# Optimization experiments

Hardware: AMD Instinct MI355X
Metric: run time of the kernel (lower is better)

## Reference

```python
import jax, jax.numpy as jnp
import numpy as np

N, E = 50000, 600000
DIMS = [128, 256, 256, 256, 256, 64]  # in, h1..h4, out


def setup_inputs() -> dict:
    key = jax.random.key(0)
    ks = jax.random.split(key, 12)
    inp = {
        "x": jax.random.normal(ks[0], (N, DIMS[0]), dtype=jnp.float32),
        "edge_index": jax.random.randint(ks[1], (2, E), 0, N, dtype=jnp.int64 if jax.config.jax_enable_x64 else jnp.int32),
    }
    for i in range(5):
        fi, fo = DIMS[i], DIMS[i + 1]
        s = 1.0 / np.sqrt(fi)  # glorot-ish uniform, matching GCNConv default scale
        inp[f"W{i+1}"] = jax.random.uniform(ks[2 + 2 * i], (fi, fo), jnp.float32, -s, s)
        inp[f"b{i+1}"] = jnp.zeros((fo,), jnp.float32)
    return inp


def _gcn_norm(edge_index, n):
    # Add self-loops and compute symmetric normalization D^-1/2 (A+I) D^-1/2.
    loop = jnp.arange(n, dtype=edge_index.dtype)
    src = jnp.concatenate([edge_index[0], loop])  # [E+N]
    dst = jnp.concatenate([edge_index[1], loop])
    deg = jax.ops.segment_sum(jnp.ones_like(dst, dtype=jnp.float32), dst, num_segments=n)
    dinv = jnp.where(deg > 0, jax.lax.rsqrt(deg), 0.0)
    norm = dinv[src] * dinv[dst]  # [E+N]
    return src, dst, norm


def _gcn_layer(x, src, dst, norm, W, b, n):
    h = x @ W                       # [N, Fo] linear transform first (fewer msg bytes)
    msg = h[src] * norm[:, None]    # gather + edge-weight scale
    out = jax.ops.segment_sum(msg, dst, num_segments=n)  # scatter-add aggregate
    return out + b


def reference(x, edge_index, W1, b1, W2, b2, W3, b3, W4, b4, W5, b5):
    n = x.shape[0]
    src, dst, norm = _gcn_norm(edge_index, n)
    params = [(W1, b1), (W2, b2), (W3, b3), (W4, b4), (W5, b5)]
    h = x
    for i, (W, b) in enumerate(params):
        h = _gcn_layer(h, src, dst, norm, W, b, n)
        if i < 4:
            h = jax.nn.relu(h)  # dropout is identity in eval mode
    return h
```

## Files before the change

kernel.cpp:

```cpp
#include <hip/hip_runtime.h>
#include <stdint.h>


typedef _Float16 v8h __attribute__((ext_vector_type(8)));
typedef float v4f __attribute__((ext_vector_type(4)));

__global__ void count_edges(const int* __restrict__ dst, int E, int* __restrict__ counts) {
    int i = blockIdx.x * blockDim.x + threadIdx.x;
    if (i < E) atomicAdd(&counts[dst[i]], 1);
}

__global__ void block_sums(const int* __restrict__ counts, int n, int* __restrict__ partial) {
    __shared__ int red[256];
    int t = threadIdx.x;
    int i = blockIdx.x * 256 + t;
    red[t] = (i < n) ? counts[i] : 0;
    __syncthreads();
    #pragma unroll
    for (int off = 128; off > 0; off >>= 1) {
        if (t < off) red[t] += red[t + off];
        __syncthreads();
    }
    if (t == 0) partial[blockIdx.x] = red[0];
}

__global__ void scan_partials(int* __restrict__ partial, int nb, int* __restrict__ row_ptr, int n) {
    __shared__ int s[256];
    int t = threadIdx.x;
    int v = (t < nb) ? partial[t] : 0;
    s[t] = v;
    __syncthreads();
    #pragma unroll
    for (int off = 1; off < 256; off <<= 1) {
        int u = (t >= off) ? s[t - off] : 0;
        __syncthreads();
        s[t] += u;
        __syncthreads();
    }
    if (t < nb) partial[t] = s[t] - v;
    if (t == 0) row_ptr[n] = s[255];
}

__global__ void scan_final(const int* __restrict__ counts, int n, const int* __restrict__ partial,
                           int* __restrict__ row_ptr, float* __restrict__ dinv,
                           int* __restrict__ fill) {
    __shared__ int s[256];
    int t = threadIdx.x;
    int i = blockIdx.x * 256 + t;
    int c = (i < n) ? counts[i] : 0;
    s[t] = c;
    __syncthreads();
    #pragma unroll
    for (int off = 1; off < 256; off <<= 1) {
        int u = (t >= off) ? s[t - off] : 0;
        __syncthreads();
        s[t] += u;
        __syncthreads();
    }
    if (i < n) {
        row_ptr[i] = partial[blockIdx.x] + s[t] - c;
        dinv[i] = rsqrtf((float)(c + 1));
        fill[i] = 0;
    }
}

__global__ void build_csr(const int* __restrict__ src, const int* __restrict__ dst, int E,
                          const int* __restrict__ row_ptr, int* __restrict__ fill,
                          int* __restrict__ ssrc, float* __restrict__ wsrc,
                          const float* __restrict__ dinv) {
    int i = blockIdx.x * blockDim.x + threadIdx.x;
    if (i < E) {
        int d = dst[i];
        int s = src[i];
        int pos = row_ptr[d] + atomicAdd(&fill[d], 1);
        ssrc[pos] = s;
        wsrc[pos] = dinv[s];
    }
}

struct SplitArgs {
    const float* W[5];
    _Float16* Wh[5];
    _Float16* Wl[5];
    int lgFI[5];
    int FO[5];
    int off[6];
};

__global__ void split_all(SplitArgs a) {
    int i = blockIdx.x * 256 + threadIdx.x;
    #pragma unroll
    for (int l = 0; l < 5; ++l) {
        if (i >= a.off[l] && i < a.off[l + 1]) {
            int j = i - a.off[l];
            int FI = 1 << a.lgFI[l];
            int c = j >> a.lgFI[l];
            int k = j & (FI - 1);
            float v = a.W[l][(size_t)k * a.FO[l] + c];
            _Float16 h = (_Float16)v;
            a.Wh[l][j] = h;
            a.Wl[l][j] = (_Float16)(v - (float)h);
        }
    }
}

template <int F, bool SPLIT_OUT>
__global__ void agg_f32(const float* __restrict__ in, const int* __restrict__ row_ptr,
                        const int* __restrict__ ssrc, const float* __restrict__ wsrc,
                        const float* __restrict__ dinv, const float* __restrict__ bias,
                        _Float16* __restrict__ outH, _Float16* __restrict__ outL,
                        float* __restrict__ outF, int n) {
    constexpr int VE = F / 64;
    int wid = (blockIdx.x * blockDim.x + threadIdx.x) >> 6;
    if (wid >= n) return;
    int lane = threadIdx.x & 63;
    const float dd = dinv[wid];
    float acc[VE];

    auto loadrow = [&](int row, float* v) {
        if constexpr (VE == 2) {
            float2 t = *(const float2*)&in[(size_t)row * F + lane * 2];
            v[0] = t.x; v[1] = t.y;
        } else {
            v[0] = in[(size_t)row * F + lane];
        }
    };

    {
        float v[VE];
        loadrow(wid, v);
        #pragma unroll
        for (int j = 0; j < VE; ++j) acc[j] = dd * v[j];
    }
    int e = row_ptr[wid];
    const int end = row_ptr[wid + 1];
    for (; e + 4 <= end; e += 4) {
        int s0 = ssrc[e], s1 = ssrc[e + 1], s2 = ssrc[e + 2], s3 = ssrc[e + 3];
        float w0 = wsrc[e], w1 = wsrc[e + 1], w2 = wsrc[e + 2], w3 = wsrc[e + 3];
        float v0[VE], v1[VE], v2[VE], v3[VE];
        loadrow(s0, v0); loadrow(s1, v1); loadrow(s2, v2); loadrow(s3, v3);
        #pragma unroll
        for (int j = 0; j < VE; ++j) acc[j] += w0 * v0[j] + w1 * v1[j];
        #pragma unroll
        for (int j = 0; j < VE; ++j) acc[j] += w2 * v2[j] + w3 * v3[j];
    }
    for (; e < end; ++e) {
        int s = ssrc[e];
        float w = wsrc[e];
        float v[VE];
        loadrow(s, v);
        #pragma unroll
        for (int j = 0; j < VE; ++j) acc[j] += w * v[j];
    }

    if constexpr (SPLIT_OUT) {
        size_t o = (size_t)wid * F + lane * VE;
        #pragma unroll
        for (int j = 0; j < VE; ++j) {
            float s = dd * acc[j];
            _Float16 h = (_Float16)s;
            outH[o + j] = h;
            outL[o + j] = (_Float16)(s - (float)h);
        }
    } else {
        #pragma unroll
        for (int j = 0; j < VE; ++j) {
            float s = dd * acc[j] + bias[lane * VE + j];
            outF[(size_t)wid * F + lane * VE + j] = s;
        }
    }
}

__global__ void agg_packed(const _Float16* __restrict__ inP, const int* __restrict__ row_ptr,
                           const int* __restrict__ ssrc, const float* __restrict__ wsrc,
                           const float* __restrict__ dinv,
                           _Float16* __restrict__ outH, _Float16* __restrict__ outL, int n) {
    int wid = (blockIdx.x * blockDim.x + threadIdx.x) >> 6;
    if (wid >= n) return;
    int lane = threadIdx.x & 63;
    const float dd = dinv[wid];
    float acc[4];

    auto loadrow = [&](int row, float* v) {
        v8h p = *(const v8h*)&inP[(size_t)row * 512 + lane * 8];
        v[0] = (float)p[0] + (float)p[1];
        v[1] = (float)p[2] + (float)p[3];
        v[2] = (float)p[4] + (float)p[5];
        v[3] = (float)p[6] + (float)p[7];
    };

    {
        float v[4];
        loadrow(wid, v);
        #pragma unroll
        for (int j = 0; j < 4; ++j) acc[j] = dd * v[j];
    }
    int e = row_ptr[wid];
    const int end = row_ptr[wid + 1];
    for (; e + 4 <= end; e += 4) {
        int s0 = ssrc[e], s1 = ssrc[e + 1], s2 = ssrc[e + 2], s3 = ssrc[e + 3];
        float w0 = wsrc[e], w1 = wsrc[e + 1], w2 = wsrc[e + 2], w3 = wsrc[e + 3];
        float v0[4], v1[4], v2[4], v3[4];
        loadrow(s0, v0); loadrow(s1, v1); loadrow(s2, v2); loadrow(s3, v3);
        #pragma unroll
        for (int j = 0; j < 4; ++j) acc[j] += w0 * v0[j] + w1 * v1[j];
        #pragma unroll
        for (int j = 0; j < 4; ++j) acc[j] += w2 * v2[j] + w3 * v3[j];
    }
    for (; e < end; ++e) {
        int s = ssrc[e];
        float w = wsrc[e];
        float v[4];
        loadrow(s, v);
        #pragma unroll
        for (int j = 0; j < 4; ++j) acc[j] += w * v[j];
    }

    size_t o = (size_t)wid * 256 + lane * 4;
    #pragma unroll
    for (int j = 0; j < 4; ++j) {
        float s = dd * acc[j];
        _Float16 h = (_Float16)s;
        outH[o + j] = h;
        outL[o + j] = (_Float16)(s - (float)h);
    }
}

__device__ __forceinline__ void gl_lds16(const _Float16* g, _Float16* l) {
    __builtin_amdgcn_global_load_lds(
        (const __attribute__((address_space(1))) uint32_t*)g,
        (__attribute__((address_space(3))) uint32_t*)l, 16, 0, 0);
}

template <int FI, int OUTMODE>
__global__ __launch_bounds__(256) void gemm_wide(
    const _Float16* __restrict__ Ah, const _Float16* __restrict__ Al,
    const _Float16* __restrict__ Wth, const _Float16* __restrict__ Wtl,
    const float* __restrict__ bias,
    uint32_t* __restrict__ Opk, _Float16* __restrict__ Oh, _Float16* __restrict__ Ol,
    int n) {
    constexpr int BK = 32;
    constexpr int NSTEP = FI / BK;
    __shared__ _Float16 lds[20480];
    const int m0 = blockIdx.x * 64;
    const int t = threadIdx.x;
    const int w = t >> 6;
    const int lane = t & 63;

    const int G = w * 64 + lane;
    const int arow = (G >> 6) * 16 + (G & 15), akc = ((G >> 4) & 3) * 8;
    const _Float16* sAh = Ah + (size_t)(m0 + arow) * FI + akc;
    const _Float16* sAl = Al + (size_t)(m0 + arow) * FI + akc;
    _Float16* dAh = &lds[w * 512];
    _Float16* dAl = &lds[2048 + w * 512];
    const int bq = lane & 15, bk = (lane >> 4) * 8;
    const _Float16* sB[4];
    _Float16* dBh[4];
    _Float16* dBl[4];
    #pragma unroll
    for (int q = 0; q < 4; ++q) {
        int sub = w * 4 + q;
        sB[q] = (const _Float16*)((size_t)(sub * 16 + bq) * FI + bk);
        dBh[q] = &lds[4096 + sub * 512];
        dBl[q] = &lds[12288 + sub * 512];
    }

    v4f acc[4][4];
    #pragma unroll
    for (int i = 0; i < 4; ++i)
        #pragma unroll
        for (int j = 0; j < 4; ++j) acc[i][j] = (v4f){0.f, 0.f, 0.f, 0.f};

    for (int s = 0; s < NSTEP; ++s) {
        const int ko = s * BK;
        gl_lds16(sAh + ko, dAh);
        gl_lds16(sAl + ko, dAl);
        #pragma unroll
        for (int q = 0; q < 4; ++q) {
            size_t off = (size_t)sB[q];
            gl_lds16(Wth + off + ko, dBh[q]);
            gl_lds16(Wtl + off + ko, dBl[q]);
        }
        __syncthreads();
        v8h ahf[4], alf[4], bhf[4], blf[4];
        #pragma unroll
        for (int i = 0; i < 4; ++i) {
            ahf[i] = *(const v8h*)&lds[i * 512 + lane * 8];
            alf[i] = *(const v8h*)&lds[2048 + i * 512 + lane * 8];
        }
        #pragma unroll
        for (int j = 0; j < 4; ++j) {
            bhf[j] = *(const v8h*)&lds[4096 + (w * 4 + j) * 512 + lane * 8];
            blf[j] = *(const v8h*)&lds[12288 + (w * 4 + j) * 512 + lane * 8];
        }
        #pragma unroll
        for (int i = 0; i < 4; ++i)
            #pragma unroll
            for (int j = 0; j < 4; ++j) {
                acc[i][j] = __builtin_amdgcn_mfma_f32_16x16x32_f16(ahf[i], bhf[j], acc[i][j], 0, 0, 0);
                acc[i][j] = __builtin_amdgcn_mfma_f32_16x16x32_f16(ahf[i], blf[j], acc[i][j], 0, 0, 0);
                acc[i][j] = __builtin_amdgcn_mfma_f32_16x16x32_f16(alf[i], bhf[j], acc[i][j], 0, 0, 0);
            }
        __syncthreads();
    }

    const int rl = (lane >> 4) * 4;
    const int cl = lane & 15;
    #pragma unroll
    for (int j = 0; j < 4; ++j) {
        const int gcol = w * 64 + j * 16 + cl;
        const float bv = bias[gcol];
        #pragma unroll
        for (int i = 0; i < 4; ++i) {
            const int grow = m0 + i * 16 + rl;
            #pragma unroll
            for (int r = 0; r < 4; ++r) {
                if (grow + r < n) {
                    float v = fmaxf(acc[i][j][r] + bv, 0.f);
                    _Float16 h = (_Float16)v;
                    _Float16 l = (_Float16)(v - (float)h);
                    if (OUTMODE == 0) {
                        uint32_t u = (uint32_t)__builtin_bit_cast(uint16_t, h) |
                                     ((uint32_t)__builtin_bit_cast(uint16_t, l) << 16);
                        Opk[(size_t)(grow + r) * 256 + gcol] = u;
                    } else {
                        Oh[(size_t)(grow + r) * 256 + gcol] = h;
                        Ol[(size_t)(grow + r) * 256 + gcol] = l;
                    }
                }
            }
        }
    }
}

__global__ __launch_bounds__(256) void gemm_narrow(
    const _Float16* __restrict__ Ah, const _Float16* __restrict__ Al,
    const _Float16* __restrict__ Wth, const _Float16* __restrict__ Wtl,
    float* __restrict__ Of, int n) {
    constexpr int FI = 256, FO = 64;
    __shared__ _Float16 lds[12288];
    const int m0 = blockIdx.x * 128;
    const int t = threadIdx.x;
    const int w = t >> 6;
    const int lane = t & 63;

    const int G0 = w * 128 + lane;
    const int G1 = G0 + 64;
    const int arow0 = (G0 >> 6) * 16 + (G0 & 15), akc0 = ((G0 >> 4) & 3) * 8;
    const int arow1 = (G1 >> 6) * 16 + (G1 & 15), akc1 = ((G1 >> 4) & 3) * 8;
    const _Float16* sAh0 = Ah + (size_t)(m0 + arow0) * FI + akc0;
    const _Float16* sAh1 = Ah + (size_t)(m0 + arow1) * FI + akc1;
    const _Float16* sAl0 = Al + (size_t)(m0 + arow0) * FI + akc0;
    const _Float16* sAl1 = Al + (size_t)(m0 + arow1) * FI + akc1;
    const int bcol = w * 16 + (lane & 15), bkc = (lane >> 4) * 8;
    const _Float16* sBh = Wth + (size_t)bcol * FI + bkc;
    const _Float16* sBl = Wtl + (size_t)bcol * FI + bkc;

    _Float16* dAh0 = &lds[w * 1024];
    _Float16* dAh1 = &lds[w * 1024 + 512];
    _Float16* dAl0 = &lds[4096 + w * 1024];
    _Float16* dAl1 = &lds[4096 + w * 1024 + 512];
    _Float16* dBh = &lds[8192 + w * 512];
    _Float16* dBl = &lds[10240 + w * 512];

    const int wm = w >> 1, wn = w & 1;
    v4f acc[4][2];
    #pragma unroll
    for (int i = 0; i < 4; ++i)
        #pragma unroll
        for (int j = 0; j < 2; ++j) acc[i][j] = (v4f){0.f, 0.f, 0.f, 0.f};

    for (int s = 0; s < 8; ++s) {
        const int ko = s * 32;
        gl_lds16(sAh0 + ko, dAh0);
        gl_lds16(sAh1 + ko, dAh1);
        gl_lds16(sAl0 + ko, dAl0);
        gl_lds16(sAl1 + ko, dAl1);
        gl_lds16(sBh + ko, dBh);
        gl_lds16(sBl + ko, dBl);
        __syncthreads();
        v8h ah[4], al[4], bh[2], bl[2];
        #pragma unroll
        for (int i = 0; i < 4; ++i) {
            ah[i] = *(const v8h*)&lds[(wm * 4 + i) * 512 + lane * 8];
            al[i] = *(const v8h*)&lds[4096 + (wm * 4 + i) * 512 + lane * 8];
        }
        #pragma unroll
        for (int j = 0; j < 2; ++j) {
            bh[j] = *(const v8h*)&lds[8192 + (wn * 2 + j) * 512 + lane * 8];
            bl[j] = *(const v8h*)&lds[10240 + (wn * 2 + j) * 512 + lane * 8];
        }
        #pragma unroll
        for (int i = 0; i < 4; ++i)
            #pragma unroll
            for (int j = 0; j < 2; ++j) {
                acc[i][j] = __builtin_amdgcn_mfma_f32_16x16x32_f16(ah[i], bh[j], acc[i][j], 0, 0, 0);
                acc[i][j] = __builtin_amdgcn_mfma_f32_16x16x32_f16(ah[i], bl[j], acc[i][j], 0, 0, 0);
                acc[i][j] = __builtin_amdgcn_mfma_f32_16x16x32_f16(al[i], bh[j], acc[i][j], 0, 0, 0);
            }
        __syncthreads();
    }

    const int rl = (lane >> 4) * 4;
    const int cl = lane & 15;
    #pragma unroll
    for (int j = 0; j < 2; ++j) {
        const int gcol = wn * 32 + j * 16 + cl;
        #pragma unroll
        for (int i = 0; i < 4; ++i) {
            const int grow = m0 + wm * 64 + i * 16 + rl;
            #pragma unroll
            for (int r = 0; r < 4; ++r)
                if (grow + r < n) Of[(size_t)(grow + r) * FO + gcol] = acc[i][j][r];
        }
    }
}

extern "C" void kernel_launch(void* const* d_in, const int* in_sizes, int n_in,
                              void* d_out, int out_size, void* d_ws, size_t ws_size,
                              hipStream_t stream) {
    const float* x = (const float*)d_in[0];
    const int* ei = (const int*)d_in[1];
    const int E = in_sizes[1] / 2;
    const int n = in_sizes[0] / 128;
    const int* esrc = ei;
    const int* edst = ei + E;
    const float* b[5] = {(const float*)d_in[3], (const float*)d_in[5], (const float*)d_in[7],
                         (const float*)d_in[9], (const float*)d_in[11]};
    float* out = (float*)d_out;
    const int NPAD = ((n + 127) / 128) * 128;

    char* ws = (char*)d_ws;
    auto carve = [&](size_t bytes) {
        char* p = ws;
        ws += (bytes + 255) & ~(size_t)255;
        return p;
    };
    int* counts = (int*)carve((size_t)n * 4);
    int* row_ptr = (int*)carve((size_t)(n + 1) * 4);
    int* fill = (int*)carve((size_t)n * 4);
    float* dinv = (float*)carve((size_t)n * 4);
    int* partial = (int*)carve(1024);
    int* ssrc = (int*)carve((size_t)E * 4);
    float* wsrc = (float*)carve((size_t)E * 4);
    const int FIs[5] = {128, 256, 256, 256, 256};
    const int FOs[5] = {256, 256, 256, 256, 64};
    _Float16 *Wh[5], *Wl[5];
    for (int l = 0; l < 5; ++l) {
        Wh[l] = (_Float16*)carve((size_t)FIs[l] * FOs[l] * 2);
        Wl[l] = (_Float16*)carve((size_t)FIs[l] * FOs[l] * 2);
    }
    _Float16* Ah = (_Float16*)carve((size_t)NPAD * 256 * 2);
    _Float16* Al = (_Float16*)carve((size_t)NPAD * 256 * 2);
    uint32_t* Ppk = (uint32_t*)carve((size_t)NPAD * 256 * 4);
    _Float16* Bh2 = (_Float16*)Ppk;
    _Float16* Bl2 = (_Float16*)Ppk + (size_t)NPAD * 256;
    float* scratch = (float*)Ah;

    hipMemsetAsync(counts, 0, (size_t)n * 4, stream);
    count_edges<<<(E + 255) / 256, 256, 0, stream>>>(edst, E, counts);
    const int nsb = (n + 255) / 256;
    block_sums<<<nsb, 256, 0, stream>>>(counts, n, partial);
    scan_partials<<<1, 256, 0, stream>>>(partial, nsb, row_ptr, n);
    scan_final<<<nsb, 256, 0, stream>>>(counts, n, partial, row_ptr, dinv, fill);
    build_csr<<<(E + 255) / 256, 256, 0, stream>>>(esrc, edst, E, row_ptr, fill, ssrc, wsrc, dinv);

    SplitArgs sa;
    int off = 0;
    for (int l = 0; l < 5; ++l) {
        sa.W[l] = (const float*)d_in[2 + 2 * l];
        sa.Wh[l] = Wh[l];
        sa.Wl[l] = Wl[l];
        sa.lgFI[l] = (FIs[l] == 128) ? 7 : 8;
        sa.FO[l] = FOs[l];
        sa.off[l] = off;
        off += FIs[l] * FOs[l];
    }
    sa.off[5] = off;
    split_all<<<(off + 255) / 256, 256, 0, stream>>>(sa);

    const int aggBlocks = (n + 3) / 4;
    const int gw = NPAD / 64;
    const int gn = NPAD / 128;

    agg_f32<128, true><<<aggBlocks, 256, 0, stream>>>(x, row_ptr, ssrc, wsrc, dinv, nullptr,
                                                      Ah, Al, nullptr, n);
    gemm_wide<128, 0><<<gw, 256, 0, stream>>>(Ah, Al, Wh[0], Wl[0], b[0], Ppk, nullptr, nullptr, n);
    for (int l = 1; l <= 2; ++l) {
        agg_packed<<<aggBlocks, 256, 0, stream>>>((const _Float16*)Ppk, row_ptr, ssrc, wsrc, dinv,
                                                  Ah, Al, n);
        gemm_wide<256, 0><<<gw, 256, 0, stream>>>(Ah, Al, Wh[l], Wl[l], b[l], Ppk, nullptr, nullptr, n);
    }
    agg_packed<<<aggBlocks, 256, 0, stream>>>((const _Float16*)Ppk, row_ptr, ssrc, wsrc, dinv,
                                              Ah, Al, n);
    gemm_wide<256, 1><<<gw, 256, 0, stream>>>(Ah, Al, Wh[3], Wl[3], b[3], nullptr, Bh2, Bl2, n);
    gemm_narrow<<<gn, 256, 0, stream>>>(Bh2, Bl2, Wh[4], Wl[4], scratch, n);
    agg_f32<64, false><<<aggBlocks, 256, 0, stream>>>(scratch, row_ptr, ssrc, wsrc, dinv, b[4],
                                                      nullptr, nullptr, out, n);
}
```

Before: 692.7 us.

## Interleave edge source and weight, unroll aggregation gathers by eight

The CSR now stores each edge's source index and its normalization weight together as one int2, so each edge needs one 8-byte load instead of two separate loads. The aggregation kernels use wave-uniform row bounds (readfirstlane), gather eight neighbor rows per iteration to keep more loads in flight, and handle the remainder with a clamped, masked group of four. Outputs are written as vector stores. The aim is more memory-level parallelism in the latency-bound gather, at the cost of higher register pressure.

```diff
diff --git a/kernel.cpp b/kernel.cpp
--- a/kernel.cpp
+++ b/kernel.cpp
@@ -3,6 +3,8 @@
 
 
 typedef _Float16 v8h __attribute__((ext_vector_type(8)));
+typedef _Float16 v4h __attribute__((ext_vector_type(4)));
+typedef _Float16 v2h __attribute__((ext_vector_type(2)));
 typedef float v4f __attribute__((ext_vector_type(4)));
 
 __global__ void count_edges(const int* __restrict__ dst, int E, int* __restrict__ counts) {
@@ -66,15 +68,13 @@
 
 __global__ void build_csr(const int* __restrict__ src, const int* __restrict__ dst, int E,
                           const int* __restrict__ row_ptr, int* __restrict__ fill,
-                          int* __restrict__ ssrc, float* __restrict__ wsrc,
-                          const float* __restrict__ dinv) {
+                          int2* __restrict__ esw, const float* __restrict__ dinv) {
     int i = blockIdx.x * blockDim.x + threadIdx.x;
     if (i < E) {
         int d = dst[i];
         int s = src[i];
         int pos = row_ptr[d] + atomicAdd(&fill[d], 1);
-        ssrc[pos] = s;
-        wsrc[pos] = dinv[s];
+        esw[pos] = make_int2(s, __float_as_int(dinv[s]));
     }
 }
 
@@ -104,126 +104,171 @@
     }
 }
 
-template <int F, bool SPLIT_OUT>
-__global__ void agg_f32(const float* __restrict__ in, const int* __restrict__ row_ptr,
-                        const int* __restrict__ ssrc, const float* __restrict__ wsrc,
-                        const float* __restrict__ dinv, const float* __restrict__ bias,
-                        _Float16* __restrict__ outH, _Float16* __restrict__ outL,
-                        float* __restrict__ outF, int n) {
-    constexpr int VE = F / 64;
+__global__ __launch_bounds__(256) void agg_packed(
+    const _Float16* __restrict__ inP, const int* __restrict__ row_ptr,
+    const int2* __restrict__ esw, const float* __restrict__ dinv,
+    _Float16* __restrict__ outH, _Float16* __restrict__ outL, int n) {
     int wid = (blockIdx.x * blockDim.x + threadIdx.x) >> 6;
     if (wid >= n) return;
-    int lane = threadIdx.x & 63;
+    const int lane = threadIdx.x & 63;
+    int e = __builtin_amdgcn_readfirstlane(row_ptr[wid]);
+    const int end = __builtin_amdgcn_readfirstlane(row_ptr[wid + 1]);
     const float dd = dinv[wid];
-    float acc[VE];
-
-    auto loadrow = [&](int row, float* v) {
-        if constexpr (VE == 2) {
-            float2 t = *(const float2*)&in[(size_t)row * F + lane * 2];
-            v[0] = t.x; v[1] = t.y;
-        } else {
-            v[0] = in[(size_t)row * F + lane];
-        }
-    };
-
+    const _Float16* rb = inP + (size_t)lane * 8;
+    float a0, a1, a2, a3;
     {
-        float v[VE];
-        loadrow(wid, v);
-        #pragma unroll
-        for (int j = 0; j < VE; ++j) acc[j] = dd * v[j];
-    }
-    int e = row_ptr[wid];
-    const int end = row_ptr[wid + 1];
-    for (; e + 4 <= end; e += 4) {
-        int s0 = ssrc[e], s1 = ssrc[e + 1], s2 = ssrc[e + 2], s3 = ssrc[e + 3];
-        float w0 = wsrc[e], w1 = wsrc[e + 1], w2 = wsrc[e + 2], w3 = wsrc[e + 3];
-        float v0[VE], v1[VE], v2[VE], v3[VE];
-        loadrow(s0, v0); loadrow(s1, v1); loadrow(s2, v2); loadrow(s3, v3);
-        #pragma unroll
-        for (int j = 0; j < VE; ++j) acc[j] += w0 * v0[j] + w1 * v1[j];
-        #pragma unroll
-        for (int j = 0; j < VE; ++j) acc[j] += w2 * v2[j] + w3 * v3[j];
-    }
-    for (; e < end; ++e) {
-        int s = ssrc[e];
-        float w = wsrc[e];
-        float v[VE];
-        loadrow(s, v);
-        #pragma unroll
-        for (int j = 0; j < VE; ++j) acc[j] += w * v[j];
-    }
-
-    if constexpr (SPLIT_OUT) {
-        size_t o = (size_t)wid * F + lane * VE;
-        #pragma unroll
-        for (int j = 0; j < VE; ++j) {
-            float s = dd * acc[j];
-            _Float16 h = (_Float16)s;
-            outH[o + j] = h;
-            outL[o + j] = (_Float16)(s - (float)h);
-        }
-    } else {
-        #pragma unroll
-        for (int j = 0; j < VE; ++j) {
-            float s = dd * acc[j] + bias[lane * VE + j];
-            outF[(size_t)wid * F + lane * VE + j] = s;
-        }
-    }
-}
-
-__global__ void agg_packed(const _Float16* __restrict__ inP, const int* __restrict__ row_ptr,
-                           const int* __restrict__ ssrc, const float* __restrict__ wsrc,
-                           const float* __restrict__ dinv,
-                           _Float16* __restrict__ outH, _Float16* __restrict__ outL, int n) {
+        v8h p = *(const v8h*)(rb + (size_t)wid * 512);
+        a0 = dd * ((float)p[0] + (float)p[1]);
+        a1 = dd * ((float)p[2] + (float)p[3]);
+        a2 = dd * ((float)p[4] + (float)p[5]);
+        a3 = dd * ((float)p[6] + (float)p[7]);
+    }
+#define GTH(q) (*(const v8h*)(rb + (size_t)(q).x * 512))
+#define ACC(b, w)                                  \
+    a0 += (w) * ((float)(b)[0] + (float)(b)[1]);   \
+    a1 += (w) * ((float)(b)[2] + (float)(b)[3]);   \
+    a2 += (w) * ((float)(b)[4] + (float)(b)[5]);   \
+    a3 += (w) * ((float)(b)[6] + (float)(b)[7]);
+    for (; e + 8 <= end; e += 8) {
+        int2 q0 = esw[e + 0], q1 = esw[e + 1], q2 = esw[e + 2], q3 = esw[e + 3];
+        int2 q4 = esw[e + 4], q5 = esw[e + 5], q6 = esw[e + 6], q7 = esw[e + 7];
+        v8h b0 = GTH(q0), b1 = GTH(q1), b2 = GTH(q2), b3 = GTH(q3);
+        v8h b4 = GTH(q4), b5 = GTH(q5), b6 = GTH(q6), b7 = GTH(q7);
+        ACC(b0, __int_as_float(q0.y)) ACC(b1, __int_as_float(q1.y))
+        ACC(b2, __int_as_float(q2.y)) ACC(b3, __int_as_float(q3.y))
+        ACC(b4, __int_as_float(q4.y)) ACC(b5, __int_as_float(q5.y))
+        ACC(b6, __int_as_float(q6.y)) ACC(b7, __int_as_float(q7.y))
+    }
+    if (e + 4 <= end) {
+        int2 q0 = esw[e + 0], q1 = esw[e + 1], q2 = esw[e + 2], q3 = esw[e + 3];
+        v8h b0 = GTH(q0), b1 = GTH(q1), b2 = GTH(q2), b3 = GTH(q3);
+        ACC(b0, __int_as_float(q0.y)) ACC(b1, __int_as_float(q1.y))
+        ACC(b2, __int_as_float(q2.y)) ACC(b3, __int_as_float(q3.y))
+        e += 4;
+    }
+    if (e < end) {
+        const int em = end - 1;
+        int e1 = (e + 1 < end) ? e + 1 : em;
+        int e2 = (e + 2 < end) ? e + 2 : em;
+        int2 q0 = esw[e], q1 = esw[e1], q2 = esw[e2], q3 = esw[em];
+        float w0 = __int_as_float(q0.y);
+        float w1 = (e + 1 < end) ? __int_as_float(q1.y) : 0.f;
+        float w2 = (e + 2 < end) ? __int_as_float(q2.y) : 0.f;
+        float w3 = (e + 3 < end) ? __int_as_float(q3.y) : 0.f;
+        v8h b0 = GTH(q0), b1 = GTH(q1), b2 = GTH(q2), b3 = GTH(q3);
+        ACC(b0, w0) ACC(b1, w1) ACC(b2, w2) ACC(b3, w3)
+    }
+#undef GTH
+#undef ACC
+    size_t o = (size_t)wid * 256 + lane * 4;
+    float s0 = dd * a0, s1 = dd * a1, s2 = dd * a2, s3 = dd * a3;
+    _Float16 h0 = (_Float16)s0, h1 = (_Float16)s1, h2 = (_Float16)s2, h3 = (_Float16)s3;
+    *(v4h*)&outH[o] = (v4h){h0, h1, h2, h3};
+    *(v4h*)&outL[o] = (v4h){(_Float16)(s0 - (float)h0), (_Float16)(s1 - (float)h1),
+                            (_Float16)(s2 - (float)h2), (_Float16)(s3 - (float)h3)};
+}
+
+__global__ __launch_bounds__(256) void agg_f32_128(
+    const float* __restrict__ in, const int* __restrict__ row_ptr,
+    const int2* __restrict__ esw, const float* __restrict__ dinv,
+    _Float16* __restrict__ outH, _Float16* __restrict__ outL, int n) {
     int wid = (blockIdx.x * blockDim.x + threadIdx.x) >> 6;
     if (wid >= n) return;
-    int lane = threadIdx.x & 63;
+    const int lane = threadIdx.x & 63;
+    int e = __builtin_amdgcn_readfirstlane(row_ptr[wid]);
+    const int end = __builtin_amdgcn_readfirstlane(row_ptr[wid + 1]);
     const float dd = dinv[wid];
-    float acc[4];
-
-    auto loadrow = [&](int row, float* v) {
-        v8h p = *(const v8h*)&inP[(size_t)row * 512 + lane * 8];
-        v[0] = (float)p[0] + (float)p[1];
-        v[1] = (float)p[2] + (float)p[3];
-        v[2] = (float)p[4] + (float)p[5];
-        v[3] = (float)p[6] + (float)p[7];
-    };
-
+    const float* rb = in + (size_t)lane * 2;
+    float a0, a1;
     {
-        float v[4];
-        loadrow(wid, v);
-        #pragma unroll
-        for (int j = 0; j < 4; ++j) acc[j] = dd * v[j];
-    }
-    int e = row_ptr[wid];
-    const int end = row_ptr[wid + 1];
-    for (; e + 4 <= end; e += 4) {
-        int s0 = ssrc[e], s1 = ssrc[e + 1], s2 = ssrc[e + 2], s3 = ssrc[e + 3];
-        float w0 = wsrc[e], w1 = wsrc[e + 1], w2 = wsrc[e + 2], w3 = wsrc[e + 3];
-        float v0[4], v1[4], v2[4], v3[4];
-        loadrow(s0, v0); loadrow(s1, v1); loadrow(s2, v2); loadrow(s3, v3);
-        #pragma unroll
-        for (int j = 0; j < 4; ++j) acc[j] += w0 * v0[j] + w1 * v1[j];
-        #pragma unroll
-        for (int j = 0; j < 4; ++j) acc[j] += w2 * v2[j] + w3 * v3[j];
-    }
-    for (; e < end; ++e) {
-        int s = ssrc[e];
-        float w = wsrc[e];
-        float v[4];
-        loadrow(s, v);
-        #pragma unroll
-        for (int j = 0; j < 4; ++j) acc[j] += w * v[j];
-    }
-
-    size_t o = (size_t)wid * 256 + lane * 4;
-    #pragma unroll
-    for (int j = 0; j < 4; ++j) {
-        float s = dd * acc[j];
-        _Float16 h = (_Float16)s;
-        outH[o + j] = h;
-        outL[o + j] = (_Float16)(s - (float)h);
-    }
+        float2 p = *(const float2*)(rb + (size_t)wid * 128);
+        a0 = dd * p.x;
+        a1 = dd * p.y;
+    }
+#define GTH(q) (*(const float2*)(rb + (size_t)(q).x * 128))
+#define ACC(b, w) a0 += (w) * (b).x; a1 += (w) * (b).y;
+    for (; e + 8 <= end; e += 8) {
+        int2 q0 = esw[e + 0], q1 = esw[e + 1], q2 = esw[e + 2], q3 = esw[e + 3];
+        int2 q4 = esw[e + 4], q5 = esw[e + 5], q6 = esw[e + 6], q7 = esw[e + 7];
+        float2 b0 = GTH(q0), b1 = GTH(q1), b2 = GTH(q2), b3 = GTH(q3);
+        float2 b4 = GTH(q4), b5 = GTH(q5), b6 = GTH(q6), b7 = GTH(q7);
+        ACC(b0, __int_as_float(q0.y)) ACC(b1, __int_as_float(q1.y))
+        ACC(b2, __int_as_float(q2.y)) ACC(b3, __int_as_float(q3.y))
+        ACC(b4, __int_as_float(q4.y)) ACC(b5, __int_as_float(q5.y))
+        ACC(b6, __int_as_float(q6.y)) ACC(b7, __int_as_float(q7.y))
+    }
+    if (e + 4 <= end) {
+        int2 q0 = esw[e + 0], q1 = esw[e + 1], q2 = esw[e + 2], q3 = esw[e + 3];
+        float2 b0 = GTH(q0), b1 = GTH(q1), b2 = GTH(q2), b3 = GTH(q3);
+        ACC(b0, __int_as_float(q0.y)) ACC(b1, __int_as_float(q1.y))
+        ACC(b2, __int_as_float(q2.y)) ACC(b3, __int_as_float(q3.y))
+        e += 4;
+    }
+    if (e < end) {
+        const int em = end - 1;
+        int e1 = (e + 1 < end) ? e + 1 : em;
+        int e2 = (e + 2 < end) ? e + 2 : em;
+        int2 q0 = esw[e], q1 = esw[e1], q2 = esw[e2], q3 = esw[em];
+        float w0 = __int_as_float(q0.y);
+        float w1 = (e + 1 < end) ? __int_as_float(q1.y) : 0.f;
+        float w2 = (e + 2 < end) ? __int_as_float(q2.y) : 0.f;
+        float w3 = (e + 3 < end) ? __int_as_float(q3.y) : 0.f;
+        float2 b0 = GTH(q0), b1 = GTH(q1), b2 = GTH(q2), b3 = GTH(q3);
+        ACC(b0, w0) ACC(b1, w1) ACC(b2, w2) ACC(b3, w3)
+    }
+#undef GTH
+#undef ACC
+    size_t o = (size_t)wid * 128 + lane * 2;
+    float s0 = dd * a0, s1 = dd * a1;
+    _Float16 h0 = (_Float16)s0, h1 = (_Float16)s1;
+    *(v2h*)&outH[o] = (v2h){h0, h1};
+    *(v2h*)&outL[o] = (v2h){(_Float16)(s0 - (float)h0), (_Float16)(s1 - (float)h1)};
+}
+
+__global__ __launch_bounds__(256) void agg_f32_64(
+    const float* __restrict__ in, const int* __restrict__ row_ptr,
+    const int2* __restrict__ esw, const float* __restrict__ dinv,
+    const float* __restrict__ bias, float* __restrict__ outF, int n) {
+    int wid = (blockIdx.x * blockDim.x + threadIdx.x) >> 6;
+    if (wid >= n) return;
+    const int lane = threadIdx.x & 63;
+    int e = __builtin_amdgcn_readfirstlane(row_ptr[wid]);
+    const int end = __builtin_amdgcn_readfirstlane(row_ptr[wid + 1]);
+    const float dd = dinv[wid];
+    const float* rb = in + lane;
+    float a0 = dd * rb[(size_t)wid * 64];
+#define GTH(q) (rb[(size_t)(q).x * 64])
+    for (; e + 8 <= end; e += 8) {
+        int2 q0 = esw[e + 0], q1 = esw[e + 1], q2 = esw[e + 2], q3 = esw[e + 3];
+        int2 q4 = esw[e + 4], q5 = esw[e + 5], q6 = esw[e + 6], q7 = esw[e + 7];
+        float b0 = GTH(q0), b1 = GTH(q1), b2 = GTH(q2), b3 = GTH(q3);
+        float b4 = GTH(q4), b5 = GTH(q5), b6 = GTH(q6), b7 = GTH(q7);
+        a0 += __int_as_float(q0.y) * b0 + __int_as_float(q1.y) * b1;
+        a0 += __int_as_float(q2.y) * b2 + __int_as_float(q3.y) * b3;
+        a0 += __int_as_float(q4.y) * b4 + __int_as_float(q5.y) * b5;
+        a0 += __int_as_float(q6.y) * b6 + __int_as_float(q7.y) * b7;
+    }
+    if (e + 4 <= end) {
+        int2 q0 = esw[e + 0], q1 = esw[e + 1], q2 = esw[e + 2], q3 = esw[e + 3];
+        float b0 = GTH(q0), b1 = GTH(q1), b2 = GTH(q2), b3 = GTH(q3);
+        a0 += __int_as_float(q0.y) * b0 + __int_as_float(q1.y) * b1;
+        a0 += __int_as_float(q2.y) * b2 + __int_as_float(q3.y) * b3;
+        e += 4;
+    }
+    if (e < end) {
+        const int em = end - 1;
+        int e1 = (e + 1 < end) ? e + 1 : em;
+        int e2 = (e + 2 < end) ? e + 2 : em;
+        int2 q0 = esw[e], q1 = esw[e1], q2 = esw[e2], q3 = esw[em];
+        float w0 = __int_as_float(q0.y);
+        float w1 = (e + 1 < end) ? __int_as_float(q1.y) : 0.f;
+        float w2 = (e + 2 < end) ? __int_as_float(q2.y) : 0.f;
+        float w3 = (e + 3 < end) ? __int_as_float(q3.y) : 0.f;
+        float b0 = GTH(q0), b1 = GTH(q1), b2 = GTH(q2), b3 = GTH(q3);
+        a0 += w0 * b0 + w1 * b1 + w2 * b2 + w3 * b3;
+    }
+#undef GTH
+    outF[(size_t)wid * 64 + lane] = dd * a0 + bias[lane];
 }
 
 __device__ __forceinline__ void gl_lds16(const _Float16* g, _Float16* l) {
@@ -441,8 +486,7 @@
     int* fill = (int*)carve((size_t)n * 4);
     float* dinv = (float*)carve((size_t)n * 4);
     int* partial = (int*)carve(1024);
-    int* ssrc = (int*)carve((size_t)E * 4);
-    float* wsrc = (float*)carve((size_t)E * 4);
+    int2* esw = (int2*)carve((size_t)E * 8);
     const int FIs[5] = {128, 256, 256, 256, 256};
     const int FOs[5] = {256, 256, 256, 256, 64};
     _Float16 *Wh[5], *Wl[5];
@@ -463,7 +507,7 @@
     block_sums<<<nsb, 256, 0, stream>>>(counts, n, partial);
     scan_partials<<<1, 256, 0, stream>>>(partial, nsb, row_ptr, n);
     scan_final<<<nsb, 256, 0, stream>>>(counts, n, partial, row_ptr, dinv, fill);
-    build_csr<<<(E + 255) / 256, 256, 0, stream>>>(esrc, edst, E, row_ptr, fill, ssrc, wsrc, dinv);
+    build_csr<<<(E + 255) / 256, 256, 0, stream>>>(esrc, edst, E, row_ptr, fill, esw, dinv);
 
     SplitArgs sa;
     int off = 0;
@@ -483,18 +527,14 @@
     const int gw = NPAD / 64;
     const int gn = NPAD / 128;
 
-    agg_f32<128, true><<<aggBlocks, 256, 0, stream>>>(x, row_ptr, ssrc, wsrc, dinv, nullptr,
-                                                      Ah, Al, nullptr, n);
+    agg_f32_128<<<aggBlocks, 256, 0, stream>>>(x, row_ptr, esw, dinv, Ah, Al, n);
     gemm_wide<128, 0><<<gw, 256, 0, stream>>>(Ah, Al, Wh[0], Wl[0], b[0], Ppk, nullptr, nullptr, n);
     for (int l = 1; l <= 2; ++l) {
-        agg_packed<<<aggBlocks, 256, 0, stream>>>((const _Float16*)Ppk, row_ptr, ssrc, wsrc, dinv,
-                                                  Ah, Al, n);
+        agg_packed<<<aggBlocks, 256, 0, stream>>>((const _Float16*)Ppk, row_ptr, esw, dinv, Ah, Al, n);
         gemm_wide<256, 0><<<gw, 256, 0, stream>>>(Ah, Al, Wh[l], Wl[l], b[l], Ppk, nullptr, nullptr, n);
     }
-    agg_packed<<<aggBlocks, 256, 0, stream>>>((const _Float16*)Ppk, row_ptr, ssrc, wsrc, dinv,
-                                              Ah, Al, n);
+    agg_packed<<<aggBlocks, 256, 0, stream>>>((const _Float16*)Ppk, row_ptr, esw, dinv, Ah, Al, n);
     gemm_wide<256, 1><<<gw, 256, 0, stream>>>(Ah, Al, Wh[3], Wl[3], b[3], nullptr, Bh2, Bl2, n);
     gemm_narrow<<<gn, 256, 0, stream>>>(Bh2, Bl2, Wh[4], Wl[4], scratch, n);
-    agg_f32<64, false><<<aggBlocks, 256, 0, stream>>>(scratch, row_ptr, ssrc, wsrc, dinv, b[4],
-                                                      nullptr, nullptr, out, n);
-}
+    agg_f32_64<<<aggBlocks, 256, 0, stream>>>(scratch, row_ptr, esw, dinv, b[4], out, n);
+}
```

New measurement: 669.5 us. 3.3% less time.
